# Optimization experiments

Measured on AMD Instinct MI355X. Metric: run time of the kernel, lower is better.

The kernel has to match this reference:

```python
import jax, jax.numpy as jnp
import numpy as np

_EPS = 1e-8

# Stacked Sobel kernels, pre-divided by 8 (matches conv2d(...)/8.0 in torch).
# Shape: (O=2, I=1, 3, 3); channel 0 = sobel_x, channel 1 = sobel_y.
_SOBEL = jnp.stack([
    jnp.array([[-1.0, 0.0, 1.0], [-2.0, 0.0, 2.0], [-1.0, 0.0, 1.0]], jnp.float32),
    jnp.array([[-1.0, -2.0, -1.0], [0.0, 0.0, 0.0], [1.0, 2.0, 1.0]], jnp.float32),
])[:, None, :, :] / 8.0


def setup_inputs() -> dict:
    key = jax.random.key(0)
    k1, k2 = jax.random.split(key)
    B, C, H, W = 64, 1, 512, 512
    pred_dist = jax.random.uniform(k1, (B, C, H, W), dtype=jnp.float32) * 10.0
    reachable = jax.random.uniform(k2, (B, C, H, W), dtype=jnp.float32)
    return {"pred_dist": pred_dist, "reachable": reachable}


def reference(pred_dist, reachable) -> jnp.ndarray:
    # Replicate (edge) padding, as F.pad(..., mode='replicate')
    padded = jnp.pad(pred_dist, ((0, 0), (0, 0), (1, 1), (1, 1)), mode="edge")
    # Single conv with 2 output channels computes grad_x and grad_y together.
    grads = jax.lax.conv_general_dilated(
        padded, _SOBEL.astype(pred_dist.dtype),
        window_strides=(1, 1), padding="VALID",
        dimension_numbers=("NCHW", "OIHW", "NCHW"),
    )  # [B, 2, H, W]
    gx = grads[:, 0:1]
    gy = grads[:, 1:2]
    magnitude = jnp.sqrt(gx * gx + gy * gy + _EPS)
    violation = jnp.abs(magnitude - 1.0)
    mask = (reachable > 0.5).astype(violation.dtype)
    denom = jnp.maximum(mask.sum(), 1.0)
    return (violation * mask).sum() / denom
```

## Files before the change

kernel.cpp:

```cpp
#include <hip/hip_runtime.h>
#include <math.h>

#define HW   512
#define IMG  (512 * 512)
#define NB   64
#define T    4
#define BLOCK 256
#define WAVES_PER_BLOCK (BLOCK / 64)
#define WAVES_PER_IMG (HW / T)
#define TOTAL_WAVES (NB * WAVES_PER_IMG)
#define NBLOCKS     (TOTAL_WAVES / WAVES_PER_BLOCK)

__device__ __forceinline__ void unpack8(const float4& q0, const float4& q1, float* a) {
    a[0] = q0.x; a[1] = q0.y; a[2] = q0.z; a[3] = q0.w;
    a[4] = q1.x; a[5] = q1.y; a[6] = q1.z; a[7] = q1.w;
}

__global__ __launch_bounds__(BLOCK, 4) void eik_main(const float* __restrict__ pred,
                                                     const float* __restrict__ reach,
                                                     float* __restrict__ partials) {
    const int lane = threadIdx.x & 63;
    const int w    = blockIdx.x * WAVES_PER_BLOCK + (threadIdx.x >> 6);
    const int y0   = (w & (WAVES_PER_IMG - 1)) * T;
    const int b    = w >> 7;
    const int xo   = lane << 3;

    const float* base = pred + (size_t)b * IMG;

    float4 P[6][2];
#pragma unroll
    for (int j = 0; j < 6; ++j) {
        int r = y0 - 1 + j;
        r = r < 0 ? 0 : (r > HW - 1 ? HW - 1 : r);
        const float* p = base + (size_t)r * HW + xo;
        P[j][0] = *(const float4*)p;
        P[j][1] = *(const float4*)(p + 4);
    }
    float4 R[T][2];
    const float* rbase = reach + (size_t)b * IMG + (size_t)y0 * HW + xo;
#pragma unroll
    for (int t = 0; t < T; ++t) {
        R[t][0] = *(const float4*)(rbase + (size_t)t * HW);
        R[t][1] = *(const float4*)(rbase + (size_t)t * HW + 4);
    }

    __builtin_amdgcn_sched_barrier(0);

    float vsum = 0.0f, csum = 0.0f;

#pragma unroll
    for (int t = 0; t < T; ++t) {
        float am[8], a0[8], ap[8], rv[8];
        unpack8(P[t][0],     P[t][1],     am);
        unpack8(P[t + 1][0], P[t + 1][1], a0);
        unpack8(P[t + 2][0], P[t + 2][1], ap);
        unpack8(R[t][0],     R[t][1],     rv);

        float s[8], d[8];
#pragma unroll
        for (int i = 0; i < 8; ++i) {
            s[i] = am[i] + 2.0f * a0[i] + ap[i];
            d[i] = ap[i] - am[i];
        }

        float sl = __shfl_up(s[7], 1, 64);
        float dl = __shfl_up(d[7], 1, 64);
        float sr = __shfl_down(s[0], 1, 64);
        float dr = __shfl_down(d[0], 1, 64);
        if (lane == 0)  { sl = s[0]; dl = d[0]; }
        if (lane == 63) { sr = s[7]; dr = d[7]; }

        const float S[10] = {sl, s[0], s[1], s[2], s[3], s[4], s[5], s[6], s[7], sr};
        const float D[10] = {dl, d[0], d[1], d[2], d[3], d[4], d[5], d[6], d[7], dr};

#pragma unroll
        for (int i = 0; i < 8; ++i) {
            const float gx = (S[i+2] - S[i]) * 0.125f;
            const float gy = (D[i] + 2.0f * D[i+1] + D[i+2]) * 0.125f;
            const float mag  = __builtin_amdgcn_sqrtf(gx * gx + gy * gy + 1e-8f);
            const float viol = fabsf(mag - 1.0f);
            const bool  m    = rv[i] > 0.5f;
            vsum += m ? viol : 0.0f;
            csum += m ? 1.0f : 0.0f;
        }
    }

#pragma unroll
    for (int off = 32; off > 0; off >>= 1) {
        vsum += __shfl_down(vsum, off, 64);
        csum += __shfl_down(csum, off, 64);
    }

    __shared__ float sv[WAVES_PER_BLOCK];
    __shared__ float sc[WAVES_PER_BLOCK];
    const int wid = threadIdx.x >> 6;
    if (lane == 0) { sv[wid] = vsum; sc[wid] = csum; }
    __syncthreads();
    if (threadIdx.x == 0) {
        partials[2 * blockIdx.x]     = sv[0] + sv[1] + sv[2] + sv[3];
        partials[2 * blockIdx.x + 1] = sc[0] + sc[1] + sc[2] + sc[3];
    }
}

__global__ __launch_bounds__(BLOCK) void eik_finalize(const float* __restrict__ partials,
                                                      float* __restrict__ out) {
    float v = 0.0f, c = 0.0f;
    for (int i = threadIdx.x; i < NBLOCKS; i += BLOCK) {
        v += partials[2 * i];
        c += partials[2 * i + 1];
    }
#pragma unroll
    for (int off = 32; off > 0; off >>= 1) {
        v += __shfl_down(v, off, 64);
        c += __shfl_down(c, off, 64);
    }
    __shared__ float sv[WAVES_PER_BLOCK];
    __shared__ float sc[WAVES_PER_BLOCK];
    const int lane = threadIdx.x & 63;
    const int wid  = threadIdx.x >> 6;
    if (lane == 0) { sv[wid] = v; sc[wid] = c; }
    __syncthreads();
    if (threadIdx.x == 0) {
        const float vt = sv[0] + sv[1] + sv[2] + sv[3];
        const float ct = sc[0] + sc[1] + sc[2] + sc[3];
        out[0] = vt / fmaxf(ct, 1.0f);
    }
}

extern "C" void kernel_launch(void* const* d_in, const int* in_sizes, int n_in,
                              void* d_out, int out_size, void* d_ws, size_t ws_size,
                              hipStream_t stream) {
    const float* pred  = (const float*)d_in[0];
    const float* reach = (const float*)d_in[1];
    float* out = (float*)d_out;
    float* ws  = (float*)d_ws;

    eik_main<<<NBLOCKS, BLOCK, 0, stream>>>(pred, reach, ws);
    eik_finalize<<<1, BLOCK, 0, stream>>>(ws, out);
}
```

Measured before the change: 143.3 us.

## Stage row strips through LDS with double-buffered async global_load_lds pipeline

Replaces direct per-wave register loads with a persistent-style block that walks 8 strips of 8 rows each. It prefetches the next strip into a second LDS buffer via global_load_lds while computing on the current one. This cuts the halo reload overhead, since overlapping 2-row halos are loaded once per strip rather than per 4-row wave, and it overlaps memory latency with compute. In exchange it uses about 72KB of LDS per block, which limits occupancy, adds barriers and hand-tuned vmcnt waits, and reduces the grid to 512 blocks.

```diff
diff --git a/kernel.cpp b/kernel.cpp
--- a/kernel.cpp
+++ b/kernel.cpp
@@ -1,88 +1,136 @@
 #include <hip/hip_runtime.h>
 #include <math.h>
 
-#define HW   512
-#define IMG  (512 * 512)
-#define NB   64
-#define T    4
+#define HW    512
+#define IMG   (512 * 512)
+#define NB    64
+#define SR    8
 #define BLOCK 256
-#define WAVES_PER_BLOCK (BLOCK / 64)
-#define WAVES_PER_IMG (HW / T)
-#define TOTAL_WAVES (NB * WAVES_PER_IMG)
-#define NBLOCKS     (TOTAL_WAVES / WAVES_PER_BLOCK)
+#define WPB   4
+#define SPB   8
+#define NBLOCKS 512
+#define PBUF(c)  ((c) * 5120)
+#define RBUF(c)  (10240 + (c) * 4096)
 
 __device__ __forceinline__ void unpack8(const float4& q0, const float4& q1, float* a) {
     a[0] = q0.x; a[1] = q0.y; a[2] = q0.z; a[3] = q0.w;
     a[4] = q1.x; a[5] = q1.y; a[6] = q1.z; a[7] = q1.w;
 }
 
-__global__ __launch_bounds__(BLOCK, 4) void eik_main(const float* __restrict__ pred,
+__device__ __forceinline__ void gload_lds16(const float* g, float* l) {
+    __builtin_amdgcn_global_load_lds(
+        (const __attribute__((address_space(1))) void*)g,
+        (__attribute__((address_space(3))) void*)l,
+        16, 0, 0);
+}
+
+__global__ __launch_bounds__(BLOCK, 2) void eik_main(const float* __restrict__ pred,
                                                      const float* __restrict__ reach,
                                                      float* __restrict__ partials) {
     const int lane = threadIdx.x & 63;
-    const int w    = blockIdx.x * WAVES_PER_BLOCK + (threadIdx.x >> 6);
-    const int y0   = (w & (WAVES_PER_IMG - 1)) * T;
-    const int b    = w >> 7;
-    const int xo   = lane << 3;
+    const int w    = threadIdx.x >> 6;
+    const int b    = blockIdx.x >> 3;
+    const int s0   = (blockIdx.x & 7) * SPB;
 
-    const float* base = pred + (size_t)b * IMG;
+    const float* pbase = pred  + (size_t)b * IMG;
+    const float* rbase = reach + (size_t)b * IMG;
 
-    float4 P[6][2];
+    __shared__ float smem[18432];
+    __shared__ float sv[WPB], sc[WPB];
+
+    auto STAGE = [&](int sl, int c) {
+        const int y0 = sl * SR;
+        float* pb = smem + PBUF(c);
+        float* rb = smem + RBUF(c);
 #pragma unroll
-    for (int j = 0; j < 6; ++j) {
-        int r = y0 - 1 + j;
-        r = r < 0 ? 0 : (r > HW - 1 ? HW - 1 : r);
-        const float* p = base + (size_t)r * HW + xo;
-        P[j][0] = *(const float4*)p;
-        P[j][1] = *(const float4*)(p + 4);
-    }
-    float4 R[T][2];
-    const float* rbase = reach + (size_t)b * IMG + (size_t)y0 * HW + xo;
-#pragma unroll
-    for (int t = 0; t < T; ++t) {
-        R[t][0] = *(const float4*)(rbase + (size_t)t * HW);
-        R[t][1] = *(const float4*)(rbase + (size_t)t * HW + 4);
-    }
-
-    __builtin_amdgcn_sched_barrier(0);
+        for (int k = 0; k < 9; ++k) {
+            const int u = (k << 2) | w;
+            if (u < 20) {
+                int gr = y0 - 1 + (u >> 1);
+                gr = gr < 0 ? 0 : (gr > HW - 1 ? HW - 1 : gr);
+                gload_lds16(pbase + (size_t)gr * HW + ((u & 1) << 8) + (lane << 2),
+                            pb + u * 256);
+            } else {
+                const int v = u - 20;
+                gload_lds16(rbase + (size_t)(y0 + (v >> 1)) * HW + ((v & 1) << 8) + (lane << 2),
+                            rb + v * 256);
+            }
+        }
+    };
 
     float vsum = 0.0f, csum = 0.0f;
 
+    STAGE(s0, 0);
+
+    for (int s = 0; s < SPB; ++s) {
+        const int cur = s & 1;
+        if (s + 1 < SPB) {
+            STAGE(s0 + s + 1, cur ^ 1);
+            asm volatile("s_waitcnt vmcnt(9)" ::: "memory");
+        } else {
+            asm volatile("s_waitcnt vmcnt(0)" ::: "memory");
+        }
+        __builtin_amdgcn_sched_barrier(0);
+        __builtin_amdgcn_s_barrier();
+        __builtin_amdgcn_sched_barrier(0);
+
+        const float* pb = smem + PBUF(cur);
+        const float* rb = smem + RBUF(cur);
+
+        float4 P[4][2], R[2][2];
 #pragma unroll
-    for (int t = 0; t < T; ++t) {
-        float am[8], a0[8], ap[8], rv[8];
-        unpack8(P[t][0],     P[t][1],     am);
-        unpack8(P[t + 1][0], P[t + 1][1], a0);
-        unpack8(P[t + 2][0], P[t + 2][1], ap);
-        unpack8(R[t][0],     R[t][1],     rv);
-
-        float s[8], d[8];
+        for (int j = 0; j < 4; ++j) {
+            const float* p = pb + (2 * w + j) * HW + (lane << 3);
+            P[j][0] = *(const float4*)p;
+            P[j][1] = *(const float4*)(p + 4);
+        }
 #pragma unroll
-        for (int i = 0; i < 8; ++i) {
-            s[i] = am[i] + 2.0f * a0[i] + ap[i];
-            d[i] = ap[i] - am[i];
+        for (int t = 0; t < 2; ++t) {
+            const float* p = rb + (2 * w + t) * HW + (lane << 3);
+            R[t][0] = *(const float4*)p;
+            R[t][1] = *(const float4*)(p + 4);
         }
 
-        float sl = __shfl_up(s[7], 1, 64);
-        float dl = __shfl_up(d[7], 1, 64);
-        float sr = __shfl_down(s[0], 1, 64);
-        float dr = __shfl_down(d[0], 1, 64);
-        if (lane == 0)  { sl = s[0]; dl = d[0]; }
-        if (lane == 63) { sr = s[7]; dr = d[7]; }
+#pragma unroll
+        for (int t = 0; t < 2; ++t) {
+            float am[8], a0[8], ap[8], rv[8];
+            unpack8(P[t][0],     P[t][1],     am);
+            unpack8(P[t + 1][0], P[t + 1][1], a0);
+            unpack8(P[t + 2][0], P[t + 2][1], ap);
+            unpack8(R[t][0],     R[t][1],     rv);
 
-        const float S[10] = {sl, s[0], s[1], s[2], s[3], s[4], s[5], s[6], s[7], sr};
-        const float D[10] = {dl, d[0], d[1], d[2], d[3], d[4], d[5], d[6], d[7], dr};
+            float sA[8], dA[8];
+#pragma unroll
+            for (int i = 0; i < 8; ++i) {
+                sA[i] = am[i] + 2.0f * a0[i] + ap[i];
+                dA[i] = ap[i] - am[i];
+            }
+
+            float sl = __shfl_up(sA[7], 1, 64);
+            float dl = __shfl_up(dA[7], 1, 64);
+            float sr = __shfl_down(sA[0], 1, 64);
+            float dr = __shfl_down(dA[0], 1, 64);
+            if (lane == 0)  { sl = sA[0]; dl = dA[0]; }
+            if (lane == 63) { sr = sA[7]; dr = dA[7]; }
+
+            const float S[10] = {sl, sA[0], sA[1], sA[2], sA[3], sA[4], sA[5], sA[6], sA[7], sr};
+            const float D[10] = {dl, dA[0], dA[1], dA[2], dA[3], dA[4], dA[5], dA[6], dA[7], dr};
 
 #pragma unroll
-        for (int i = 0; i < 8; ++i) {
-            const float gx = (S[i+2] - S[i]) * 0.125f;
-            const float gy = (D[i] + 2.0f * D[i+1] + D[i+2]) * 0.125f;
-            const float mag  = __builtin_amdgcn_sqrtf(gx * gx + gy * gy + 1e-8f);
-            const float viol = fabsf(mag - 1.0f);
-            const bool  m    = rv[i] > 0.5f;
-            vsum += m ? viol : 0.0f;
-            csum += m ? 1.0f : 0.0f;
+            for (int i = 0; i < 8; ++i) {
+                const float gx = (S[i+2] - S[i]) * 0.125f;
+                const float gy = (D[i] + 2.0f * D[i+1] + D[i+2]) * 0.125f;
+                const float mag  = __builtin_amdgcn_sqrtf(gx * gx + gy * gy + 1e-8f);
+                const float viol = fabsf(mag - 1.0f);
+                const bool  m    = rv[i] > 0.5f;
+                vsum += m ? viol : 0.0f;
+                csum += m ? 1.0f : 0.0f;
+            }
         }
+
+        __builtin_amdgcn_sched_barrier(0);
+        __builtin_amdgcn_s_barrier();
+        __builtin_amdgcn_sched_barrier(0);
     }
 
 #pragma unroll
@@ -90,11 +138,7 @@
         vsum += __shfl_down(vsum, off, 64);
         csum += __shfl_down(csum, off, 64);
     }
-
-    __shared__ float sv[WAVES_PER_BLOCK];
-    __shared__ float sc[WAVES_PER_BLOCK];
-    const int wid = threadIdx.x >> 6;
-    if (lane == 0) { sv[wid] = vsum; sc[wid] = csum; }
+    if (lane == 0) { sv[w] = vsum; sc[w] = csum; }
     __syncthreads();
     if (threadIdx.x == 0) {
         partials[2 * blockIdx.x]     = sv[0] + sv[1] + sv[2] + sv[3];
@@ -114,8 +158,7 @@
         v += __shfl_down(v, off, 64);
         c += __shfl_down(c, off, 64);
     }
-    __shared__ float sv[WAVES_PER_BLOCK];
-    __shared__ float sc[WAVES_PER_BLOCK];
+    __shared__ float sv[4], sc[4];
     const int lane = threadIdx.x & 63;
     const int wid  = threadIdx.x >> 6;
     if (lane == 0) { sv[wid] = v; sc[wid] = c; }
```

Result: slower. 151.1 us (+5.5%).

## Process eight rows per wave with rolling software-pipelined row loads

Applied to the files above, without the earlier changes.

Doubles rows per wave from four to eight and replaces the up-front bulk load of all rows with a rolling three-row window. The next row of pred and reach is prefetched one iteration ahead, and the scheduling barrier is removed. This cuts halo re-reads between vertically adjacent waves and lowers register pressure. In exchange it halves the number of waves and blocks, and leaves fewer loads in flight per wave, which may expose memory latency.

```diff
diff --git a/kernel.cpp b/kernel.cpp
--- a/kernel.cpp
+++ b/kernel.cpp
@@ -4,7 +4,7 @@
 #define HW   512
 #define IMG  (512 * 512)
 #define NB   64
-#define T    4
+#define T    8
 #define BLOCK 256
 #define WAVES_PER_BLOCK (BLOCK / 64)
 #define WAVES_PER_IMG (HW / T)
@@ -22,39 +22,49 @@
     const int lane = threadIdx.x & 63;
     const int w    = blockIdx.x * WAVES_PER_BLOCK + (threadIdx.x >> 6);
     const int y0   = (w & (WAVES_PER_IMG - 1)) * T;
-    const int b    = w >> 7;
+    const int b    = w / WAVES_PER_IMG;
     const int xo   = lane << 3;
 
-    const float* base = pred + (size_t)b * IMG;
+    const float* base  = pred  + (size_t)b * IMG;
+    const float* rbase = reach + (size_t)b * IMG;
 
-    float4 P[6][2];
-#pragma unroll
-    for (int j = 0; j < 6; ++j) {
-        int r = y0 - 1 + j;
-        r = r < 0 ? 0 : (r > HW - 1 ? HW - 1 : r);
-        const float* p = base + (size_t)r * HW + xo;
-        P[j][0] = *(const float4*)p;
-        P[j][1] = *(const float4*)(p + 4);
+    auto rowp = [&](int y) {
+        y = y < 0 ? 0 : (y > HW - 1 ? HW - 1 : y);
+        return base + (size_t)y * HW + xo;
+    };
+
+    float4 am0, am1, a00, a01, ap0, ap1;
+    {
+        const float* p = rowp(y0 - 1);
+        am0 = *(const float4*)p; am1 = *(const float4*)(p + 4);
+        p = rowp(y0);
+        a00 = *(const float4*)p; a01 = *(const float4*)(p + 4);
+        p = rowp(y0 + 1);
+        ap0 = *(const float4*)p; ap1 = *(const float4*)(p + 4);
     }
-    float4 R[T][2];
-    const float* rbase = reach + (size_t)b * IMG + (size_t)y0 * HW + xo;
-#pragma unroll
-    for (int t = 0; t < T; ++t) {
-        R[t][0] = *(const float4*)(rbase + (size_t)t * HW);
-        R[t][1] = *(const float4*)(rbase + (size_t)t * HW + 4);
+    float4 rv0, rv1;
+    {
+        const float* p = rbase + (size_t)y0 * HW + xo;
+        rv0 = *(const float4*)p; rv1 = *(const float4*)(p + 4);
     }
-
-    __builtin_amdgcn_sched_barrier(0);
 
     float vsum = 0.0f, csum = 0.0f;
 
 #pragma unroll
     for (int t = 0; t < T; ++t) {
+        float4 nx0, nx1, rn0, rn1;
+        if (t < T - 1) {
+            const float* p = rowp(y0 + t + 2);
+            nx0 = *(const float4*)p; nx1 = *(const float4*)(p + 4);
+            p = rbase + (size_t)(y0 + t + 1) * HW + xo;
+            rn0 = *(const float4*)p; rn1 = *(const float4*)(p + 4);
+        }
+
         float am[8], a0[8], ap[8], rv[8];
-        unpack8(P[t][0],     P[t][1],     am);
-        unpack8(P[t + 1][0], P[t + 1][1], a0);
-        unpack8(P[t + 2][0], P[t + 2][1], ap);
-        unpack8(R[t][0],     R[t][1],     rv);
+        unpack8(am0, am1, am);
+        unpack8(a00, a01, a0);
+        unpack8(ap0, ap1, ap);
+        unpack8(rv0, rv1, rv);
 
         float s[8], d[8];
 #pragma unroll
@@ -83,6 +93,11 @@
             vsum += m ? viol : 0.0f;
             csum += m ? 1.0f : 0.0f;
         }
+
+        am0 = a00; am1 = a01;
+        a00 = ap0; a01 = ap1;
+        ap0 = nx0; ap1 = nx1;
+        rv0 = rn0; rv1 = rn1;
     }
 
 #pragma unroll
```

New measurement: 145.9 us. No clear change (+1.8%).
